# Kernel tuning notes

Hardware: AMD Instinct MI355X
Metric: run time of the kernel (lower is better)

Reference implementation:

```python
import jax, jax.numpy as jnp
import numpy as np

EMBED_DIM = 1024
HEADS = 16
HEAD_DIM = EMBED_DIM // HEADS


def setup_inputs() -> dict:
    key = jax.random.key(0)
    ks = jax.random.split(key, 12)
    B, Sq, Sk, E = 4, 2048, 2048, EMBED_DIM
    s = 1.0 / np.sqrt(E)
    return {
        "query": jax.random.normal(ks[0], (B, Sq, E), jnp.float32),
        "key": jax.random.normal(ks[1], (B, Sk, E), jnp.float32),
        "value": jax.random.normal(ks[2], (B, Sk, E), jnp.float32),
        "Wq": jax.random.normal(ks[3], (E, E), jnp.float32) * s,
        "bq": jnp.zeros((E,), jnp.float32),
        "Wk": jax.random.normal(ks[4], (E, E), jnp.float32) * s,
        "bk": jnp.zeros((E,), jnp.float32),
        "Wv": jax.random.normal(ks[5], (E, E), jnp.float32) * s,
        "bv": jnp.zeros((E,), jnp.float32),
        "Wo": jax.random.normal(ks[6], (E, E), jnp.float32) * s,
        "bo": jnp.zeros((E,), jnp.float32),
    }


def reference(query, key, value, Wq, bq, Wk, bk, Wv, bv, Wo, bo):
    B, Sq, E = query.shape
    Sk = key.shape[1]
    H, D = HEADS, HEAD_DIM
    # projections -> [B, H, S, D]
    Q = (query @ Wq + bq).reshape(B, Sq, H, D).transpose(0, 2, 1, 3)
    K = (key @ Wk + bk).reshape(B, Sk, H, D).transpose(0, 2, 1, 3)
    V = (value @ Wv + bv).reshape(B, Sk, H, D).transpose(0, 2, 1, 3)
    scores = jnp.einsum('bhqd,bhkd->bhqk', Q, K) / jnp.sqrt(jnp.float32(D))
    attn = jax.nn.softmax(scores, axis=-1)
    out = jnp.einsum('bhqk,bhkd->bhqd', attn, V)  # [B,H,Sq,D]
    out = out.transpose(0, 2, 1, 3).reshape(B, Sq, E)
    return out @ Wo + bo
```

## Files before the change

### kernel.cpp

```cpp
#include <hip/hip_runtime.h>
#include <hip/hip_bf16.h>
#include <cstdint>
#include <cstddef>

#define EDIM 1024
#define HEADS 16
#define HD 64
#define BATCH 4
#define SQ 2048
#define SK 2048
#define MROWS (BATCH * SQ)

typedef __bf16 bf16;
typedef __bf16 bf16x8 __attribute__((ext_vector_type(8)));
typedef float f32x4 __attribute__((ext_vector_type(4)));

#define GLDS16(gp, lp)                                                        \
  __builtin_amdgcn_global_load_lds(                                           \
      (const __attribute__((address_space(1))) void*)(gp),                    \
      (__attribute__((address_space(3))) void*)(lp), 16, 0, 0)

__device__ __forceinline__ int swz(int row, int col) {
  return row * 64 + (col ^ ((row & 7) << 3));
}

__global__ __launch_bounds__(256) void cast_bf16_kernel(
    const float* __restrict__ in, bf16* __restrict__ out) {
  int t = blockIdx.x * 256 + threadIdx.x;
  const float4* p = (const float4*)(in + (size_t)t * 8);
  float4 a = p[0], b = p[1];
  bf16x8 o;
  o[0] = (bf16)a.x; o[1] = (bf16)a.y; o[2] = (bf16)a.z; o[3] = (bf16)a.w;
  o[4] = (bf16)b.x; o[5] = (bf16)b.y; o[6] = (bf16)b.z; o[7] = (bf16)b.w;
  *(bf16x8*)(out + (size_t)t * 8) = o;
}

__global__ __launch_bounds__(256) void transcast_kernel(
    const float* __restrict__ W, bf16* __restrict__ Wt) {
  __shared__ float tile[64][65];
  const int t = threadIdx.x;
  const int k0 = blockIdx.x * 64, n0 = blockIdx.y * 64;
  const int c = t & 63, r4 = t >> 6;
#pragma unroll
  for (int i = 0; i < 16; ++i) {
    int kr = i * 4 + r4;
    tile[kr][c] = W[(size_t)(k0 + kr) * EDIM + n0 + c];
  }
  __syncthreads();
#pragma unroll
  for (int i = 0; i < 16; ++i) {
    int nr = i * 4 + r4;
    Wt[(size_t)(n0 + nr) * EDIM + k0 + c] = (bf16)tile[c][nr];
  }
}

template <int MODE>
__global__ __launch_bounds__(256) void gemm_nt_kernel(
    const bf16* __restrict__ A, const bf16* __restrict__ Bt,
    const float* __restrict__ bias, void* __restrict__ out) {
  __shared__ bf16 As[128 * 64];
  __shared__ bf16 Bs[128 * 64];
  const int tid = threadIdx.x;
  const int w = tid >> 6, lane = tid & 63;
  const int wr = w >> 1, wc = w & 1;
  const int m0 = blockIdx.x * 128, n0 = blockIdx.y * 128;
  const int lr = lane >> 3;
  const int lc = (lane & 7) * 8;

  f32x4 acc[4][4] = {};

  for (int kt = 0; kt < EDIM; kt += 64) {
#pragma unroll
    for (int i = 0; i < 4; ++i) {
      int r = w * 32 + i * 8;
      GLDS16(A + (size_t)(m0 + r + lr) * EDIM + kt + lc, &As[r * 64]);
      GLDS16(Bt + (size_t)(n0 + r + lr) * EDIM + kt + lc, &Bs[r * 64]);
    }
    __syncthreads();
#pragma unroll
    for (int ks = 0; ks < 2; ++ks) {
      bf16x8 af[4], bfr[4];
#pragma unroll
      for (int i = 0; i < 4; ++i) {
        af[i]  = *(const bf16x8*)&As[(wr * 64 + i * 16 + (lane & 15)) * 64 +
                                     ks * 32 + (lane >> 4) * 8];
        bfr[i] = *(const bf16x8*)&Bs[(wc * 64 + i * 16 + (lane & 15)) * 64 +
                                     ks * 32 + (lane >> 4) * 8];
      }
#pragma unroll
      for (int mi = 0; mi < 4; ++mi)
#pragma unroll
        for (int ni = 0; ni < 4; ++ni)
          acc[mi][ni] = __builtin_amdgcn_mfma_f32_16x16x32_bf16(
              af[mi], bfr[ni], acc[mi][ni], 0, 0, 0);
    }
    __syncthreads();
  }

#pragma unroll
  for (int mi = 0; mi < 4; ++mi)
#pragma unroll
    for (int ni = 0; ni < 4; ++ni)
#pragma unroll
      for (int r = 0; r < 4; ++r) {
        int row = m0 + wr * 64 + mi * 16 + (lane >> 4) * 4 + r;
        int col = n0 + wc * 64 + ni * 16 + (lane & 15);
        float v = acc[mi][ni][r] + bias[col];
        if (MODE == 0) {
          int b = row >> 11, s = row & 2047, h = col >> 6, d = col & 63;
          ((bf16*)out)[(((size_t)(b * HEADS + h) * SQ) + s) * HD + d] = (bf16)v;
        } else if (MODE == 2) {
          int b = row >> 11, s = row & 2047, h = col >> 6, d = col & 63;
          ((bf16*)out)[(((size_t)(b * HEADS + h) * HD) + d) * SK + s] = (bf16)v;
        } else {
          ((float*)out)[(size_t)row * EDIM + col] = v;
        }
      }
}

__global__ __launch_bounds__(256) void attn_kernel(
    const bf16* __restrict__ Qh, const bf16* __restrict__ Kh,
    const bf16* __restrict__ VTh, bf16* __restrict__ Ao) {
  __shared__ bf16 Qs[64 * 64];
  __shared__ bf16 Ks[64 * 64];
  __shared__ bf16 Vs[64 * 64];
  __shared__ bf16 Ps[64 * 64];
  const int tid = threadIdx.x, w = tid >> 6, lane = tid & 63;
  const int bh = blockIdx.y;
  const int q0 = blockIdx.x * 64;
  const int lr = lane >> 3;
  const int lcs = ((lane & 7) ^ (lane >> 3)) * 8;
  const float LOG2E = 1.44269504088896f;

#pragma unroll
  for (int i = 0; i < 2; ++i) {
    int r = w * 16 + i * 8;
    GLDS16(Qh + ((size_t)bh * SQ + q0 + r + lr) * HD + lcs, &Qs[r * 64]);
  }
  __syncthreads();
  bf16x8 qf[2];
  qf[0] = *(const bf16x8*)&Qs[swz(w * 16 + (lane & 15), (lane >> 4) * 8)];
  qf[1] = *(const bf16x8*)&Qs[swz(w * 16 + (lane & 15), 32 + (lane >> 4) * 8)];

  float mrow[4] = {-1e30f, -1e30f, -1e30f, -1e30f};
  float lsum[4] = {0.f, 0.f, 0.f, 0.f};
  f32x4 oacc[4] = {};

  for (int kc = 0; kc < SK; kc += 64) {
    __syncthreads();
#pragma unroll
    for (int i = 0; i < 2; ++i) {
      int r = w * 16 + i * 8;
      GLDS16(Kh + ((size_t)bh * SK + kc + r + lr) * HD + lcs, &Ks[r * 64]);
      GLDS16(VTh + ((size_t)bh * HD + r + lr) * SK + kc + lcs, &Vs[r * 64]);
    }
    __syncthreads();

    f32x4 s[4];
#pragma unroll
    for (int ct = 0; ct < 4; ++ct) {
      bf16x8 kf0 = *(const bf16x8*)&Ks[swz(ct * 16 + (lane & 15), (lane >> 4) * 8)];
      bf16x8 kf1 = *(const bf16x8*)&Ks[swz(ct * 16 + (lane & 15), 32 + (lane >> 4) * 8)];
      f32x4 t = {};
      __builtin_amdgcn_s_setprio(1);
      t = __builtin_amdgcn_mfma_f32_16x16x32_bf16(qf[0], kf0, t, 0, 0, 0);
      t = __builtin_amdgcn_mfma_f32_16x16x32_bf16(qf[1], kf1, t, 0, 0, 0);
      __builtin_amdgcn_s_setprio(0);
      s[ct] = t;
    }

    float pv[4][4];
    float esc[4];
#pragma unroll
    for (int r = 0; r < 4; ++r) {
      float mx = -1e30f;
#pragma unroll
      for (int ct = 0; ct < 4; ++ct) {
        float v = s[ct][r] * 0.125f;
        pv[ct][r] = v;
        mx = fmaxf(mx, v);
      }
#pragma unroll
      for (int m = 1; m < 16; m <<= 1) mx = fmaxf(mx, __shfl_xor(mx, m));
      float mnew = fmaxf(mrow[r], mx);
      esc[r] = exp2f((mrow[r] - mnew) * LOG2E);
      mrow[r] = mnew;
      float sum = 0.f;
#pragma unroll
      for (int ct = 0; ct < 4; ++ct) {
        float p = exp2f((pv[ct][r] - mnew) * LOG2E);
        pv[ct][r] = p;
        sum += p;
      }
#pragma unroll
      for (int m = 1; m < 16; m <<= 1) sum += __shfl_xor(sum, m);
      lsum[r] = lsum[r] * esc[r] + sum;
    }
#pragma unroll
    for (int dt = 0; dt < 4; ++dt)
#pragma unroll
      for (int r = 0; r < 4; ++r) oacc[dt][r] *= esc[r];

    bf16* Pw = &Ps[w * 16 * 64];
#pragma unroll
    for (int ct = 0; ct < 4; ++ct)
#pragma unroll
      for (int r = 0; r < 4; ++r)
        Pw[swz((lane >> 4) * 4 + r, ct * 16 + (lane & 15))] = (bf16)pv[ct][r];
    asm volatile("s_waitcnt lgkmcnt(0)" ::: "memory");
    __builtin_amdgcn_sched_barrier(0);

    bf16x8 pf0 = *(const bf16x8*)&Pw[swz(lane & 15, (lane >> 4) * 8)];
    bf16x8 pf1 = *(const bf16x8*)&Pw[swz(lane & 15, 32 + (lane >> 4) * 8)];
#pragma unroll
    for (int dt = 0; dt < 4; ++dt) {
      bf16x8 vf0 = *(const bf16x8*)&Vs[swz(dt * 16 + (lane & 15), (lane >> 4) * 8)];
      bf16x8 vf1 = *(const bf16x8*)&Vs[swz(dt * 16 + (lane & 15), 32 + (lane >> 4) * 8)];
      __builtin_amdgcn_s_setprio(1);
      oacc[dt] = __builtin_amdgcn_mfma_f32_16x16x32_bf16(pf0, vf0, oacc[dt], 0, 0, 0);
      oacc[dt] = __builtin_amdgcn_mfma_f32_16x16x32_bf16(pf1, vf1, oacc[dt], 0, 0, 0);
      __builtin_amdgcn_s_setprio(0);
    }
  }

  int b = bh >> 4, h = bh & 15;
#pragma unroll
  for (int r = 0; r < 4; ++r) {
    float inv = 1.0f / lsum[r];
    int q = q0 + w * 16 + (lane >> 4) * 4 + r;
#pragma unroll
    for (int dt = 0; dt < 4; ++dt) {
      int d = dt * 16 + (lane & 15);
      Ao[((size_t)(b * SQ + q)) * EDIM + h * HD + d] = (bf16)(oacc[dt][r] * inv);
    }
  }
}

extern "C" void kernel_launch(void* const* d_in, const int* in_sizes, int n_in,
                              void* d_out, int out_size, void* d_ws,
                              size_t ws_size, hipStream_t stream) {
  const float* query = (const float*)d_in[0];
  const float* key   = (const float*)d_in[1];
  const float* value = (const float*)d_in[2];
  const float* Wq = (const float*)d_in[3];
  const float* bq = (const float*)d_in[4];
  const float* Wk = (const float*)d_in[5];
  const float* bk = (const float*)d_in[6];
  const float* Wv = (const float*)d_in[7];
  const float* bv = (const float*)d_in[8];
  const float* Wo = (const float*)d_in[9];
  const float* bo = (const float*)d_in[10];

  char* ws = (char*)d_ws;
  bf16* headQ  = (bf16*)(ws);
  bf16* headK  = (bf16*)(ws + (16ull << 20));
  bf16* headVT = (bf16*)(ws + (32ull << 20));
  bf16* WqT = (bf16*)(ws + (48ull << 20));
  bf16* WkT = (bf16*)(ws + (50ull << 20));
  bf16* WvT = (bf16*)(ws + (52ull << 20));
  bf16* WoT = (bf16*)(ws + (54ull << 20));
  bf16* Xq  = (bf16*)(ws + (56ull << 20));
  bf16* Xk  = (bf16*)(ws + (72ull << 20));
  bf16* Xv  = (bf16*)(ws + (88ull << 20));
  bf16* attnb = Xq;

  cast_bf16_kernel<<<4096, 256, 0, stream>>>(query, Xq);
  cast_bf16_kernel<<<4096, 256, 0, stream>>>(key, Xk);
  cast_bf16_kernel<<<4096, 256, 0, stream>>>(value, Xv);
  dim3 gt(EDIM / 64, EDIM / 64);
  transcast_kernel<<<gt, 256, 0, stream>>>(Wq, WqT);
  transcast_kernel<<<gt, 256, 0, stream>>>(Wk, WkT);
  transcast_kernel<<<gt, 256, 0, stream>>>(Wv, WvT);
  transcast_kernel<<<gt, 256, 0, stream>>>(Wo, WoT);

  dim3 gg(MROWS / 128, EDIM / 128);
  gemm_nt_kernel<0><<<gg, 256, 0, stream>>>(Xq, WqT, bq, headQ);
  gemm_nt_kernel<0><<<gg, 256, 0, stream>>>(Xk, WkT, bk, headK);
  gemm_nt_kernel<2><<<gg, 256, 0, stream>>>(Xv, WvT, bv, headVT);

  dim3 ga(SQ / 64, BATCH * HEADS);
  attn_kernel<<<ga, 256, 0, stream>>>(headQ, headK, headVT, attnb);

  gemm_nt_kernel<3><<<gg, 256, 0, stream>>>(attnb, WoT, bo, d_out);
}
```

Measured before the change: 519.0 us.

## Compute softmax row sums via MFMA, prescale Q, and stage V-transpose stores

The attention kernel now folds the 1/sqrt(D) scale into the Q fragments once, and replaces the per-row shuffle reduction of exp sums with an extra MFMA against a ones vector. It then reads the row sums back with a single shuffle at the end. The V projection GEMM (MODE 2) stages its output tile transposed in shared memory and writes 16-byte vectorized rows instead of scattered 2-byte strided stores. Risks include bf16 rounding of the scaled Q and of P inside the row-sum accumulation, which slightly changes numerics, plus extra LDS use in the MODE 2 GEMM.

New measurement: 476.6 us. -8.2%, faster.

```diff
diff --git a/kernel.cpp b/kernel.cpp
--- a/kernel.cpp
+++ b/kernel.cpp
@@ -58,8 +58,9 @@
 __global__ __launch_bounds__(256) void gemm_nt_kernel(
     const bf16* __restrict__ A, const bf16* __restrict__ Bt,
     const float* __restrict__ bias, void* __restrict__ out) {
-  __shared__ bf16 As[128 * 64];
-  __shared__ bf16 Bs[128 * 64];
+  __shared__ __align__(16) bf16 smem[(MODE == 2) ? (128 * 136) : (2 * 128 * 64)];
+  bf16* As = smem;
+  bf16* Bs = smem + 128 * 64;
   const int tid = threadIdx.x;
   const int w = tid >> 6, lane = tid & 63;
   const int wr = w >> 1, wc = w & 1;
@@ -95,6 +96,31 @@
               af[mi], bfr[ni], acc[mi][ni], 0, 0, 0);
     }
     __syncthreads();
+  }
+
+  if (MODE == 2) {
+#pragma unroll
+    for (int mi = 0; mi < 4; ++mi)
+#pragma unroll
+      for (int ni = 0; ni < 4; ++ni)
+#pragma unroll
+        for (int r = 0; r < 4; ++r) {
+          int sl = wr * 64 + mi * 16 + (lane >> 4) * 4 + r;
+          int cl = wc * 64 + ni * 16 + (lane & 15);
+          smem[cl * 136 + sl] = (bf16)(acc[mi][ni][r] + bias[n0 + cl]);
+        }
+    __syncthreads();
+    const int b = m0 >> 11, sbase = m0 & 2047;
+    const int s0 = (tid & 15) * 8;
+#pragma unroll
+    for (int i = 0; i < 8; ++i) {
+      int cl = (tid >> 4) + i * 16;
+      int cg = n0 + cl, h = cg >> 6, d = cg & 63;
+      bf16x8 v = *(const bf16x8*)&smem[cl * 136 + s0];
+      *(bf16x8*)((bf16*)out +
+                 ((size_t)(b * HEADS + h) * HD + d) * SK + sbase + s0) = v;
+    }
+    return;
   }
 
 #pragma unroll
@@ -109,9 +135,6 @@
         if (MODE == 0) {
           int b = row >> 11, s = row & 2047, h = col >> 6, d = col & 63;
           ((bf16*)out)[(((size_t)(b * HEADS + h) * SQ) + s) * HD + d] = (bf16)v;
-        } else if (MODE == 2) {
-          int b = row >> 11, s = row & 2047, h = col >> 6, d = col & 63;
-          ((bf16*)out)[(((size_t)(b * HEADS + h) * HD) + d) * SK + s] = (bf16)v;
         } else {
           ((float*)out)[(size_t)row * EDIM + col] = v;
         }
@@ -141,10 +164,21 @@
   bf16x8 qf[2];
   qf[0] = *(const bf16x8*)&Qs[swz(w * 16 + (lane & 15), (lane >> 4) * 8)];
   qf[1] = *(const bf16x8*)&Qs[swz(w * 16 + (lane & 15), 32 + (lane >> 4) * 8)];
+#pragma unroll
+  for (int i = 0; i < 2; ++i)
+#pragma unroll
+    for (int j = 0; j < 8; ++j) qf[i][j] = (bf16)((float)qf[i][j] * 0.125f);
+
+  bf16x8 onesf;
+  {
+    bf16 o1 = (lane & 15) == 0 ? (bf16)1.0f : (bf16)0.0f;
+#pragma unroll
+    for (int j = 0; j < 8; ++j) onesf[j] = o1;
+  }
 
   float mrow[4] = {-1e30f, -1e30f, -1e30f, -1e30f};
-  float lsum[4] = {0.f, 0.f, 0.f, 0.f};
   f32x4 oacc[4] = {};
+  f32x4 oaccS = {};
 
   for (int kc = 0; kc < SK; kc += 64) {
     __syncthreads();
@@ -176,30 +210,24 @@
       float mx = -1e30f;
 #pragma unroll
       for (int ct = 0; ct < 4; ++ct) {
-        float v = s[ct][r] * 0.125f;
-        pv[ct][r] = v;
-        mx = fmaxf(mx, v);
+        pv[ct][r] = s[ct][r];
+        mx = fmaxf(mx, s[ct][r]);
       }
 #pragma unroll
       for (int m = 1; m < 16; m <<= 1) mx = fmaxf(mx, __shfl_xor(mx, m));
       float mnew = fmaxf(mrow[r], mx);
       esc[r] = exp2f((mrow[r] - mnew) * LOG2E);
       mrow[r] = mnew;
-      float sum = 0.f;
-#pragma unroll
-      for (int ct = 0; ct < 4; ++ct) {
-        float p = exp2f((pv[ct][r] - mnew) * LOG2E);
-        pv[ct][r] = p;
-        sum += p;
-      }
-#pragma unroll
-      for (int m = 1; m < 16; m <<= 1) sum += __shfl_xor(sum, m);
-      lsum[r] = lsum[r] * esc[r] + sum;
+#pragma unroll
+      for (int ct = 0; ct < 4; ++ct)
+        pv[ct][r] = exp2f((pv[ct][r] - mnew) * LOG2E);
     }
 #pragma unroll
     for (int dt = 0; dt < 4; ++dt)
 #pragma unroll
       for (int r = 0; r < 4; ++r) oacc[dt][r] *= esc[r];
+#pragma unroll
+    for (int r = 0; r < 4; ++r) oaccS[r] *= esc[r];
 
     bf16* Pw = &Ps[w * 16 * 64];
 #pragma unroll
@@ -221,12 +249,17 @@
       oacc[dt] = __builtin_amdgcn_mfma_f32_16x16x32_bf16(pf1, vf1, oacc[dt], 0, 0, 0);
       __builtin_amdgcn_s_setprio(0);
     }
+    __builtin_amdgcn_s_setprio(1);
+    oaccS = __builtin_amdgcn_mfma_f32_16x16x32_bf16(pf0, onesf, oaccS, 0, 0, 0);
+    oaccS = __builtin_amdgcn_mfma_f32_16x16x32_bf16(pf1, onesf, oaccS, 0, 0, 0);
+    __builtin_amdgcn_s_setprio(0);
   }
 
   int b = bh >> 4, h = bh & 15;
 #pragma unroll
   for (int r = 0; r < 4; ++r) {
-    float inv = 1.0f / lsum[r];
+    float l = __shfl(oaccS[r], lane & 48);
+    float inv = 1.0f / l;
     int q = q0 + w * 16 + (lane >> 4) * 4 + r;
 #pragma unroll
     for (int dt = 0; dt < 4; ++dt) {
```
